# Performance work log

Hardware: AMD Instinct MI355X
Metric: run time of the kernel (lower is better)

## Reference

```python
import jax, jax.numpy as jnp
import numpy as np

GRID_SIZE = 5
SPLINE_ORDER = 3
GRID_RANGE = (-1.0, 1.0)
LAYERS = [1024, 1024, 1024]
BATCH = 8192
LN_EPS = 1e-5


def _make_grid(in_features):
    h = (GRID_RANGE[1] - GRID_RANGE[0]) / GRID_SIZE
    n = GRID_SIZE + 2 * SPLINE_ORDER + 1  # 12 knots
    g = jnp.linspace(GRID_RANGE[0] - h * SPLINE_ORDER,
                     GRID_RANGE[1] + h * SPLINE_ORDER, n, dtype=jnp.float32)
    return jnp.broadcast_to(g, (in_features, n))


def setup_inputs() -> dict:
    key = jax.random.key(0)
    ks = jax.random.split(key, 8)
    n_layers = len(LAYERS) - 1
    d_in, d_out = LAYERS[0], LAYERS[1]  # square layers -> stackable params
    coeff = GRID_SIZE + SPLINE_ORDER  # 8
    # kaiming_uniform_(nonlinearity='linear'): bound = sqrt(3) * (1/sqrt(fan_in))
    bw_bound = float(np.sqrt(3.0) / np.sqrt(d_in))
    sw_bound = float(np.sqrt(3.0) / np.sqrt(d_in * coeff))
    x = jax.random.normal(ks[0], (BATCH, d_in), dtype=jnp.float32)
    base_w = jax.random.uniform(ks[1], (n_layers, d_out, d_in), jnp.float32, -bw_bound, bw_bound)
    spline_w = jax.random.uniform(ks[2], (n_layers, d_out, d_in, coeff), jnp.float32, -sw_bound, sw_bound)
    ln_g = jnp.ones((n_layers, d_out), jnp.float32)
    ln_b = jnp.zeros((n_layers, d_out), jnp.float32)
    prelu_a = jnp.full((n_layers,), 0.25, jnp.float32)
    grid = jnp.stack([_make_grid(d_in) for _ in range(n_layers)])  # [L, in, 12]
    return {"x": x, "base_w": base_w, "spline_w": spline_w,
            "ln_g": ln_g, "ln_b": ln_b, "prelu_a": prelu_a, "grid": grid}


def _bspline_bases(x, g):
    """Cox-de Boor recursion. x: [B, in], g: [in, n_knots] -> [B, in, G+order]."""
    xu = x[..., None]  # [B, in, 1]
    bases = ((xu >= g[:, :-1]) & (xu < g[:, 1:])).astype(x.dtype)  # [B, in, 11]
    for k in range(1, SPLINE_ORDER + 1):
        left = g[:, :-(k + 1)]
        right = g[:, k:-1]
        delta = jnp.where(right == left, jnp.ones_like(right), right - left)
        bases = ((xu - left) / delta * bases[..., :-1]
                 + (g[:, k + 1:] - xu) / (g[:, k + 1:] - g[:, 1:-k]) * bases[..., 1:])
    return bases  # [B, in, 8]


def kan_forward(x, base_w, spline_w, ln_g, ln_b, prelu_a, grid):
    n_layers = base_w.shape[0]
    for i in range(n_layers):
        base_out = jnp.matmul(jax.nn.gelu(x, approximate=False), base_w[i].T)  # [B, out]
        bases = _bspline_bases(x, grid[i])  # [B, in, 8]
        spline_out = jnp.matmul(bases.reshape(x.shape[0], -1),
                                spline_w[i].reshape(spline_w.shape[1], -1).T)  # [B, out]
        h = base_out + spline_out
        mu = jnp.mean(h, axis=-1, keepdims=True)
        var = jnp.var(h, axis=-1, keepdims=True)  # biased, matches torch LayerNorm
        h = (h - mu) * jax.lax.rsqrt(var + LN_EPS) * ln_g[i] + ln_b[i]
        x = jnp.where(h >= 0, h, prelu_a[i] * h)  # PReLU (scalar slope per layer)
    return x


def reference(x, base_w, spline_w, ln_g, ln_b, prelu_a, grid):
    return kan_forward(x, base_w, spline_w, ln_g, ln_b, prelu_a, grid)
```

## Files before the change

### kernel.cpp

```cpp
#include <hip/hip_runtime.h>
#include <hip/hip_bf16.h>
#include <cstdint>
#include <cstddef>

typedef __bf16 bf16_t;
typedef __bf16 bf16x8 __attribute__((ext_vector_type(8)));
typedef __bf16 bf16x4 __attribute__((ext_vector_type(4)));
typedef float  f32x4  __attribute__((ext_vector_type(4)));

#define DIM    1024
#define NCOEF  8
#define KTOT   (DIM + DIM * NCOEF)
#define NKNOT  12
#define BATCH  8192
#define LN_EPS 1e-5f

__device__ __forceinline__ float gelu_exact(float x) {
    return 0.5f * x * (1.0f + erff(x * 0.70710678118654752440f));
}

__device__ __forceinline__ void gl_lds16(const void* g, void* l) {
    __builtin_amdgcn_global_load_lds(
        (const __attribute__((address_space(1))) unsigned int*)(uintptr_t)g,
        (__attribute__((address_space(3))) unsigned int*)(uintptr_t)l, 16, 0, 0);
}

__device__ __forceinline__ uint64_t pack4bf(float a, float b, float c, float d) {
    union { bf16_t h[4]; uint64_t q; } u;
    u.h[0] = (bf16_t)a; u.h[1] = (bf16_t)b; u.h[2] = (bf16_t)c; u.h[3] = (bf16_t)d;
    return u.q;
}

__device__ __forceinline__ void spline8(float x, float g0, float invh,
                                        uint64_t& lo, uint64_t& hi) {
    float u = (x - g0) * invh;
    float jf = floorf(u);
    int j = (int)jf;
    float f = u - jf;
    float f2 = f * f, f3 = f2 * f;
    float om = 1.0f - f, om2 = om * om;
    float w0 = om2 * om * (1.0f / 6.0f);
    float w3 = f3 * (1.0f / 6.0f);
    float w1 = fmaf(0.5f, f3, 2.0f / 3.0f) - f2;
    float w2 = 1.0f - w0 - w1 - w3;
    uint64_t W64 = pack4bf(w0, w1, w2, w3);
    if (!(u >= 0.0f && u < 11.0f)) W64 = 0;
    int sh = (j - 3) * 16;
    if (sh >= 0) {
        int s = sh & 63;
        uint64_t loW = W64 << s;
        uint64_t hiW = s ? (W64 >> (64 - s)) : 0ull;
        lo = (sh < 64) ? loW : 0ull;
        hi = (sh < 64) ? hiW : loW;
    } else {
        lo = W64 >> (-sh);
        hi = 0ull;
    }
}

__global__ void pack_w(const float* __restrict__ bw, const float* __restrict__ sw,
                       bf16_t* __restrict__ W) {
    int idx = blockIdx.x * 256 + threadIdx.x;
    bf16_t* wrow = W + (size_t)(idx >> 10) * KTOT;
    int j = idx & 1023;
    wrow[j] = (bf16_t)bw[idx];
    const float4* sp = (const float4*)(sw + (size_t)idx * NCOEF);
    float4 s0 = sp[0], s1 = sp[1];
    bf16x8 v;
    v[0] = (bf16_t)s0.x; v[1] = (bf16_t)s0.y; v[2] = (bf16_t)s0.z; v[3] = (bf16_t)s0.w;
    v[4] = (bf16_t)s1.x; v[5] = (bf16_t)s1.y; v[6] = (bf16_t)s1.z; v[7] = (bf16_t)s1.w;
    *(bf16x8*)(wrow + DIM + j * NCOEF) = v;
}

__global__ void prep_A(const float* __restrict__ x, bf16_t* __restrict__ A,
                       const float* __restrict__ gp, int R) {
    const int t = threadIdx.x;
    const float g0 = gp[0];
    const float invh = 1.0f / (gp[1] - gp[0]);
    for (int row = blockIdx.x; row < R; row += gridDim.x) {
        f32x4 v = *(const f32x4*)(x + (size_t)row * DIM + t * 4);
        bf16_t* Ar = A + (size_t)row * KTOT;
        bf16x4 ge;
#pragma unroll
        for (int k = 0; k < 4; k++) ge[k] = (bf16_t)gelu_exact(v[k]);
        *(bf16x4*)(Ar + t * 4) = ge;
#pragma unroll
        for (int k = 0; k < 4; k++) {
            uint64_t lo, hi;
            union { uint64_t u[2]; uint4 q; } o;
            spline8(v[k], g0, invh, lo, hi);
            o.u[0] = lo; o.u[1] = hi;
            *(uint4*)(Ar + DIM + (t * 4 + k) * NCOEF) = o.q;
        }
    }
}


#define STR2(x) #x
#define GATEV(N) asm volatile("s_waitcnt vmcnt(" STR2(N) ")" ::: "memory");
#define LGKM(N)  asm volatile("s_waitcnt lgkmcnt(" STR2(N) ")" ::: "memory");
#define BAR() { __builtin_amdgcn_s_barrier(); asm volatile("" ::: "memory"); }

#define EA(i) ea##i
#define EB(i) eb##i
#define OA(i) oa##i
#define OB(i) ob##i

#define MF_ROWX(I, A_, CB) \
    acc[I][0] = __builtin_amdgcn_mfma_f32_16x16x32_bf16(A_, CB(0), acc[I][0], 0, 0, 0); \
    acc[I][1] = __builtin_amdgcn_mfma_f32_16x16x32_bf16(A_, CB(1), acc[I][1], 0, 0, 0); \
    acc[I][2] = __builtin_amdgcn_mfma_f32_16x16x32_bf16(A_, CB(2), acc[I][2], 0, 0, 0); \
    acc[I][3] = __builtin_amdgcn_mfma_f32_16x16x32_bf16(A_, CB(3), acc[I][3], 0, 0, 0);

#define TILE(T, S, SN, SP, STG, GATESTMT, RD, WAITB, CA, CB, NA, NB) { \
     \
    if (STG) { \
      gl_lds16(Ag0 + (size_t)((T) + 3) * 32, ldsA + (SP) * 8192 + tid * 8); \
      gl_lds16(Ag1 + (size_t)((T) + 3) * 32, ldsA + (SP) * 8192 + 4096 + tid * 8); } \
    { const bf16_t* Ab_ = ldsA + (S) * 8192 + aOff; \
      CA(4) = *(const bf16x8*)(Ab_ + 2048); CA(5) = *(const bf16x8*)(Ab_ + 2560); \
      CA(6) = *(const bf16x8*)(Ab_ + 3072); CA(7) = *(const bf16x8*)(Ab_ + 3584); } \
    LGKM(4) \
    __builtin_amdgcn_sched_barrier(0); \
    __builtin_amdgcn_s_setprio(1); \
    MF_ROWX(0, CA(0), CB) MF_ROWX(1, CA(1), CB) \
    MF_ROWX(2, CA(2), CB) MF_ROWX(3, CA(3), CB) \
    __builtin_amdgcn_s_setprio(0); \
     \
    if (STG) { \
      gl_lds16(Bg0 + (size_t)((T) + 3) * 32, ldsB + (SP) * 8192 + tid * 8); \
      gl_lds16(Bg1 + (size_t)((T) + 3) * 32, ldsB + (SP) * 8192 + 4096 + tid * 8); } \
    GATESTMT \
    if (RD) { \
      BAR() \
      const bf16_t* An_ = ldsA + (SN) * 8192 + aOff; \
      const bf16_t* Bn_ = ldsB + (SN) * 8192 + bOff; \
      NA(0) = *(const bf16x8*)(An_);        NA(1) = *(const bf16x8*)(An_ + 512); \
      NA(2) = *(const bf16x8*)(An_ + 1024); NA(3) = *(const bf16x8*)(An_ + 1536); \
      NB(0) = *(const bf16x8*)(Bn_);        NB(1) = *(const bf16x8*)(Bn_ + 512); \
      NB(2) = *(const bf16x8*)(Bn_ + 1024); NB(3) = *(const bf16x8*)(Bn_ + 1536); } \
    WAITB \
    __builtin_amdgcn_sched_barrier(0); \
    __builtin_amdgcn_s_setprio(1); \
    MF_ROWX(4, CA(4), CB) MF_ROWX(5, CA(5), CB) \
    MF_ROWX(6, CA(6), CB) MF_ROWX(7, CA(7), CB) \
    __builtin_amdgcn_s_setprio(0); \
    BAR() \
}

#define PSTAGE(T, S) \
    gl_lds16(Ag0 + (size_t)(T) * 32, ldsA + (S) * 8192 + tid * 8); \
    gl_lds16(Ag1 + (size_t)(T) * 32, ldsA + (S) * 8192 + 4096 + tid * 8); \
    gl_lds16(Bg0 + (size_t)(T) * 32, ldsB + (S) * 8192 + tid * 8); \
    gl_lds16(Bg1 + (size_t)(T) * 32, ldsB + (S) * 8192 + 4096 + tid * 8);

template<int NTK>
__global__ __launch_bounds__(512, 2) void gemm_ab(
    const bf16_t* __restrict__ A,
    const bf16_t* __restrict__ W,
    float* __restrict__ C,
    int mmask, int mshift, int rows) {
    __shared__ __align__(16) bf16_t lds[65536];
    bf16_t* __restrict__ ldsA = lds;
    bf16_t* __restrict__ ldsB = lds + 32768;

    const int tid = threadIdx.x;
    const int l = tid & 63, wv = tid >> 6;
    const int wm = wv >> 2, wn = wv & 3;

    const int chunk = gridDim.x >> 3;
    const int bid = blockIdx.x;
    const int wg = (bid & 7) * chunk + (bid >> 3);
    const int bm = wg & mmask;
    const int bn = (wg >> mshift) & 3;
    const int ks = wg >> (mshift + 2);
    const int row0 = bm << 8, col0 = bn << 8;
    const int koff0 = ks * (NTK * 32);

    const int srow = tid >> 2;
    const int slc = (tid & 3) ^ ((srow >> 1) & 3);
    const bf16_t* __restrict__ Ag0 = A + (size_t)(row0 + srow) * KTOT + koff0 + slc * 8;
    const bf16_t* __restrict__ Ag1 = Ag0 + (size_t)128 * KTOT;
    const bf16_t* __restrict__ Bg0 = W + (size_t)(col0 + srow) * KTOT + koff0 + slc * 8;
    const bf16_t* __restrict__ Bg1 = Bg0 + (size_t)128 * KTOT;

    const int l15 = l & 15;
    const int pc = (l >> 4) ^ ((l15 >> 1) & 3);
    const int aOff = (wm * 128 + l15) * 32 + pc * 8;
    const int bOff = (wn * 64 + l15) * 32 + pc * 8;

    f32x4 acc[8][4] = {};
    bf16x8 ea0, ea1, ea2, ea3, ea4, ea5, ea6, ea7, eb0, eb1, eb2, eb3;
    bf16x8 oa0, oa1, oa2, oa3, oa4, oa5, oa6, oa7, ob0, ob1, ob2, ob3;

    PSTAGE(0, 0)
    PSTAGE(1, 1)
    PSTAGE(2, 2)
    GATEV(8)
    BAR()
    {
        const bf16_t* An_ = ldsA + aOff;
        const bf16_t* Bn_ = ldsB + bOff;
        ea0 = *(const bf16x8*)(An_);        ea1 = *(const bf16x8*)(An_ + 512);
        ea2 = *(const bf16x8*)(An_ + 1024); ea3 = *(const bf16x8*)(An_ + 1536);
        eb0 = *(const bf16x8*)(Bn_);        eb1 = *(const bf16x8*)(Bn_ + 512);
        eb2 = *(const bf16x8*)(Bn_ + 1024); eb3 = *(const bf16x8*)(Bn_ + 1536);
    }

#pragma unroll 1
    for (int t = 0; t < NTK - 4; t += 4) {
        TILE(t + 0, 0, 1, 3, 1, GATEV(8), 1, LGKM(8), EA, EB, OA, OB)
        TILE(t + 1, 1, 2, 0, 1, GATEV(8), 1, LGKM(8), OA, OB, EA, EB)
        TILE(t + 2, 2, 3, 1, 1, GATEV(8), 1, LGKM(8), EA, EB, OA, OB)
        TILE(t + 3, 3, 0, 2, 1, GATEV(8), 1, LGKM(8), OA, OB, EA, EB)
    }
    TILE(NTK - 4, 0, 1, 3, 1, GATEV(8), 1, LGKM(8), EA, EB, OA, OB)
    TILE(NTK - 3, 1, 2, 0, 0, GATEV(4), 1, LGKM(8), OA, OB, EA, EB)
    TILE(NTK - 2, 2, 3, 1, 0, GATEV(0), 1, LGKM(8), EA, EB, OA, OB)
    TILE(NTK - 1, 3, 0, 2, 0, GATEV(0), 0, LGKM(0), OA, OB, EA, EB)

    float* __restrict__ Cp = C + (size_t)ks * rows * DIM;
    const int r0 = row0 + wm * 128 + (l >> 4) * 4;
    const int c0 = col0 + wn * 64 + l15;
#pragma unroll
    for (int i = 0; i < 8; i++)
#pragma unroll
        for (int j = 0; j < 4; j++)
#pragma unroll
            for (int r = 0; r < 4; r++)
                Cp[(size_t)(r0 + i * 16 + r) * DIM + c0 + j * 16] = acc[i][j][r];
}

__global__ void ln_mid_A(const float* __restrict__ h, int rows, int ksplit,
                         const float* __restrict__ g_ln, const float* __restrict__ b_ln,
                         const float* __restrict__ pa, bf16_t* __restrict__ A,
                         const float* __restrict__ gp) {
    const int tid = threadIdx.x;
    const int w = tid >> 6, l = tid & 63;
    const float a = pa[0];
    const float g0 = gp[0];
    const float invh = 1.0f / (gp[1] - gp[0]);
    __shared__ float rs[4], rq[4];
    for (int row = blockIdx.x; row < rows; row += gridDim.x) {
        f32x4 v = {0.0f, 0.0f, 0.0f, 0.0f};
        for (int ks = 0; ks < ksplit; ks++)
            v += *(const f32x4*)(h + ((size_t)ks * rows + row) * DIM + tid * 4);
        float s = v[0] + v[1] + v[2] + v[3];
        float q = v[0] * v[0] + v[1] * v[1] + v[2] * v[2] + v[3] * v[3];
#pragma unroll
        for (int o = 32; o > 0; o >>= 1) { s += __shfl_xor(s, o); q += __shfl_xor(q, o); }
        if (l == 0) { rs[w] = s; rq[w] = q; }
        __syncthreads();
        s = rs[0] + rs[1] + rs[2] + rs[3];
        q = rq[0] + rq[1] + rq[2] + rq[3];
        __syncthreads();
        float mean = s * (1.0f / DIM);
        float var = q * (1.0f / DIM) - mean * mean;
        float rstd = rsqrtf(var + LN_EPS);
        bf16_t* Ar = A + (size_t)row * KTOT;
        bf16x4 ge;
#pragma unroll
        for (int c = 0; c < 4; c++) {
            int col = tid * 4 + c;
            float yv = (v[c] - mean) * rstd * g_ln[col] + b_ln[col];
            yv = (yv >= 0.0f) ? yv : a * yv;
            ge[c] = (bf16_t)gelu_exact(yv);
            uint64_t lo, hi;
            union { uint64_t u[2]; uint4 qv; } o;
            spline8(yv, g0, invh, lo, hi);
            o.u[0] = lo; o.u[1] = hi;
            *(uint4*)(Ar + DIM + (size_t)col * NCOEF) = o.qv;
        }
        *(bf16x4*)(Ar + tid * 4) = ge;
    }
}

__global__ void ln_out(const float* __restrict__ h, int rows, int ksplit,
                       const float* __restrict__ g_ln, const float* __restrict__ b_ln,
                       const float* __restrict__ pa, float* __restrict__ out) {
    const int tid = threadIdx.x;
    const int w = tid >> 6, l = tid & 63;
    const float a = pa[0];
    __shared__ float rs[4], rq[4];
    for (int row = blockIdx.x; row < rows; row += gridDim.x) {
        f32x4 v = {0.0f, 0.0f, 0.0f, 0.0f};
        for (int ks = 0; ks < ksplit; ks++)
            v += *(const f32x4*)(h + ((size_t)ks * rows + row) * DIM + tid * 4);
        float s = v[0] + v[1] + v[2] + v[3];
        float q = v[0] * v[0] + v[1] * v[1] + v[2] * v[2] + v[3] * v[3];
#pragma unroll
        for (int o = 32; o > 0; o >>= 1) { s += __shfl_xor(s, o); q += __shfl_xor(q, o); }
        if (l == 0) { rs[w] = s; rq[w] = q; }
        __syncthreads();
        s = rs[0] + rs[1] + rs[2] + rs[3];
        q = rq[0] + rq[1] + rq[2] + rq[3];
        __syncthreads();
        float mean = s * (1.0f / DIM);
        float var = q * (1.0f / DIM) - mean * mean;
        float rstd = rsqrtf(var + LN_EPS);
        f32x4 o4;
#pragma unroll
        for (int c = 0; c < 4; c++) {
            int col = tid * 4 + c;
            float yv = (v[c] - mean) * rstd * g_ln[col] + b_ln[col];
            o4[c] = (yv >= 0.0f) ? yv : a * yv;
        }
        *(f32x4*)(out + (size_t)row * DIM + tid * 4) = o4;
    }
}

extern "C" void kernel_launch(void* const* d_in, const int* in_sizes, int n_in,
                              void* d_out, int out_size, void* d_ws, size_t ws_size,
                              hipStream_t stream) {
    const float* x    = (const float*)d_in[0];
    const float* bw   = (const float*)d_in[1];
    const float* sw   = (const float*)d_in[2];
    const float* ln_g = (const float*)d_in[3];
    const float* ln_b = (const float*)d_in[4];
    const float* pa   = (const float*)d_in[5];
    const float* gridK = (const float*)d_in[6];
    float* out = (float*)d_out;

    const size_t wbytes = (size_t)2 * DIM * KTOT * sizeof(bf16_t);
    int R = 8192, ksplit = 2;
    for (;;) {
        size_t need = wbytes + (size_t)R * KTOT * 2 + (size_t)ksplit * R * DIM * 4;
        if (need <= ws_size || R == 512) break;
        R >>= 1;
        int mt = R / 256;
        ksplit = (mt >= 32) ? 2 : (mt >= 16) ? 4 : 8;
    }
    int mtiles = R / 256;
    int mshift = 0; while ((1 << mshift) < mtiles) mshift++;
    int mmask = mtiles - 1;
    int grid = mtiles * 4 * ksplit;
    int lng = (R >= 2048) ? 2048 : R;

    char* wsc = (char*)d_ws;
    bf16_t* Wbuf = (bf16_t*)wsc;
    bf16_t* Abuf = (bf16_t*)(wsc + wbytes);
    float*  hbuf = (float*)(wsc + wbytes + (size_t)R * KTOT * 2);

    pack_w<<<(2 * DIM * DIM) / 256, 256, 0, stream>>>(bw, sw, Wbuf);

    auto launch_gemm = [&](const bf16_t* Wl, hipStream_t st) {
        if (ksplit == 2)
            gemm_ab<144><<<grid, 512, 0, st>>>(Abuf, Wl, hbuf, mmask, mshift, R);
        else if (ksplit == 4)
            gemm_ab<72><<<grid, 512, 0, st>>>(Abuf, Wl, hbuf, mmask, mshift, R);
        else
            gemm_ab<36><<<grid, 512, 0, st>>>(Abuf, Wl, hbuf, mmask, mshift, R);
    };

    const int nslab = BATCH / R;
    for (int sidx = 0; sidx < nslab; sidx++) {
        const size_t row0 = (size_t)sidx * R;
        const float* x0 = x + row0 * DIM;
        prep_A<<<lng, 256, 0, stream>>>(x0, Abuf, gridK, R);
        launch_gemm(Wbuf, stream);
        ln_mid_A<<<lng, 256, 0, stream>>>(hbuf, R, ksplit, ln_g, ln_b, pa,
                                          Abuf, gridK + DIM * NKNOT);
        launch_gemm(Wbuf + (size_t)DIM * KTOT, stream);
        ln_out<<<lng, 256, 0, stream>>>(hbuf, R, ksplit, ln_g + DIM, ln_b + DIM,
                                        pa + 1, out + row0 * DIM);
    }
}
```

Baseline: 574.8 us.

## Restructure GEMM main loop into K=64 double-buffered 8-phase ping-pong schedule

```diff
diff --git a/kernel.cpp b/kernel.cpp
--- a/kernel.cpp
+++ b/kernel.cpp
@@ -98,61 +98,78 @@
 
 #define STR2(x) #x
 #define GATEV(N) asm volatile("s_waitcnt vmcnt(" STR2(N) ")" ::: "memory");
-#define LGKM(N)  asm volatile("s_waitcnt lgkmcnt(" STR2(N) ")" ::: "memory");
+#define LGKM0    asm volatile("s_waitcnt lgkmcnt(0)" ::: "memory");
 #define BAR() { __builtin_amdgcn_s_barrier(); asm volatile("" ::: "memory"); }
 
-#define EA(i) ea##i
-#define EB(i) eb##i
-#define OA(i) oa##i
-#define OB(i) ob##i
-
-#define MF_ROWX(I, A_, CB) \
-    acc[I][0] = __builtin_amdgcn_mfma_f32_16x16x32_bf16(A_, CB(0), acc[I][0], 0, 0, 0); \
-    acc[I][1] = __builtin_amdgcn_mfma_f32_16x16x32_bf16(A_, CB(1), acc[I][1], 0, 0, 0); \
-    acc[I][2] = __builtin_amdgcn_mfma_f32_16x16x32_bf16(A_, CB(2), acc[I][2], 0, 0, 0); \
-    acc[I][3] = __builtin_amdgcn_mfma_f32_16x16x32_bf16(A_, CB(3), acc[I][3], 0, 0, 0);
-
-#define TILE(T, S, SN, SP, STG, GATESTMT, RD, WAITB, CA, CB, NA, NB) { \
-     \
-    if (STG) { \
-      gl_lds16(Ag0 + (size_t)((T) + 3) * 32, ldsA + (SP) * 8192 + tid * 8); \
-      gl_lds16(Ag1 + (size_t)((T) + 3) * 32, ldsA + (SP) * 8192 + 4096 + tid * 8); } \
-    { const bf16_t* Ab_ = ldsA + (S) * 8192 + aOff; \
-      CA(4) = *(const bf16x8*)(Ab_ + 2048); CA(5) = *(const bf16x8*)(Ab_ + 2560); \
-      CA(6) = *(const bf16x8*)(Ab_ + 3072); CA(7) = *(const bf16x8*)(Ab_ + 3584); } \
-    LGKM(4) \
-    __builtin_amdgcn_sched_barrier(0); \
-    __builtin_amdgcn_s_setprio(1); \
-    MF_ROWX(0, CA(0), CB) MF_ROWX(1, CA(1), CB) \
-    MF_ROWX(2, CA(2), CB) MF_ROWX(3, CA(3), CB) \
-    __builtin_amdgcn_s_setprio(0); \
-     \
-    if (STG) { \
-      gl_lds16(Bg0 + (size_t)((T) + 3) * 32, ldsB + (SP) * 8192 + tid * 8); \
-      gl_lds16(Bg1 + (size_t)((T) + 3) * 32, ldsB + (SP) * 8192 + 4096 + tid * 8); } \
-    GATESTMT \
-    if (RD) { \
-      BAR() \
-      const bf16_t* An_ = ldsA + (SN) * 8192 + aOff; \
-      const bf16_t* Bn_ = ldsB + (SN) * 8192 + bOff; \
-      NA(0) = *(const bf16x8*)(An_);        NA(1) = *(const bf16x8*)(An_ + 512); \
-      NA(2) = *(const bf16x8*)(An_ + 1024); NA(3) = *(const bf16x8*)(An_ + 1536); \
-      NB(0) = *(const bf16x8*)(Bn_);        NB(1) = *(const bf16x8*)(Bn_ + 512); \
-      NB(2) = *(const bf16x8*)(Bn_ + 1024); NB(3) = *(const bf16x8*)(Bn_ + 1536); } \
-    WAITB \
-    __builtin_amdgcn_sched_barrier(0); \
-    __builtin_amdgcn_s_setprio(1); \
-    MF_ROWX(4, CA(4), CB) MF_ROWX(5, CA(5), CB) \
-    MF_ROWX(6, CA(6), CB) MF_ROWX(7, CA(7), CB) \
-    __builtin_amdgcn_s_setprio(0); \
-    BAR() \
-}
-
-#define PSTAGE(T, S) \
-    gl_lds16(Ag0 + (size_t)(T) * 32, ldsA + (S) * 8192 + tid * 8); \
-    gl_lds16(Ag1 + (size_t)(T) * 32, ldsA + (S) * 8192 + 4096 + tid * 8); \
-    gl_lds16(Bg0 + (size_t)(T) * 32, ldsB + (S) * 8192 + tid * 8); \
-    gl_lds16(Bg1 + (size_t)(T) * 32, ldsB + (S) * 8192 + 4096 + tid * 8);
+#define RD_A(DST, BO, G) { \
+    const bf16_t* p_ = ldsA + (BO) + aOffBase + (G) * 2048; \
+    DST[0][0] = *(const bf16x8*)(p_);        DST[1][0] = *(const bf16x8*)(p_ + 512); \
+    DST[2][0] = *(const bf16x8*)(p_ + 1024); DST[3][0] = *(const bf16x8*)(p_ + 1536); \
+    DST[0][1] = *(const bf16x8*)(p_ + 4096); DST[1][1] = *(const bf16x8*)(p_ + 4608); \
+    DST[2][1] = *(const bf16x8*)(p_ + 5120); DST[3][1] = *(const bf16x8*)(p_ + 5632); }
+
+#define RD_B(DST, BO, CG) { \
+    const bf16_t* p_ = ldsB + (BO) + bOffBase + (CG) * 1024; \
+    DST[0][0] = *(const bf16x8*)(p_);        DST[1][0] = *(const bf16x8*)(p_ + 512); \
+    DST[0][1] = *(const bf16x8*)(p_ + 4096); DST[1][1] = *(const bf16x8*)(p_ + 4608); }
+
+#define STG_A(TILE, HALF) { \
+    const bf16_t* s_ = AgS + (size_t)(HALF) * (128 * (size_t)KTOT) + (size_t)(TILE) * 64; \
+    bf16_t* d_ = ldsA + (((TILE) & 1) * 16384) + (HALF) * 8192 + tid * 8; \
+    gl_lds16(s_, d_); gl_lds16(s_ + 32, d_ + 4096); }
+
+#define STG_B(TILE, HALF) { \
+    const bf16_t* s_ = BgS + (size_t)(HALF) * (128 * (size_t)KTOT) + (size_t)(TILE) * 64; \
+    bf16_t* d_ = ldsB + (((TILE) & 1) * 16384) + (HALF) * 8192 + tid * 8; \
+    gl_lds16(s_, d_); gl_lds16(s_ + 32, d_ + 4096); }
+
+#define MFQ(G, CG, AS, BS) { \
+    _Pragma("unroll") \
+    for (int ks_ = 0; ks_ < 2; ks_++) \
+    _Pragma("unroll") \
+    for (int fr_ = 0; fr_ < 4; fr_++) \
+    _Pragma("unroll") \
+    for (int cf_ = 0; cf_ < 2; cf_++) \
+        acc[(G) * 4 + fr_][(CG) * 2 + cf_] = __builtin_amdgcn_mfma_f32_16x16x32_bf16( \
+            AS[fr_][ks_], BS[cf_][ks_], acc[(G) * 4 + fr_][(CG) * 2 + cf_], 0, 0, 0); }
+
+#define PHX(MF, ENDG) \
+    BAR() LGKM0 __builtin_amdgcn_sched_barrier(0); \
+    __builtin_amdgcn_s_setprio(1); MF __builtin_amdgcn_s_setprio(0); \
+    ENDG BAR()
+
+#define ITER8(T, S12, S34, S56, S78, G4T, G8T) { \
+     \
+    RD_A(Ar0, 0, 0) RD_B(Bc0, 0, 0) \
+    if (S12) { STG_B((T) + 1, 0) } \
+    PHX(MFQ(0, 0, Ar0, Bc0), ;) \
+     \
+    RD_A(Ar1, 0, 1) \
+    if (S12) { STG_B((T) + 1, 1) } \
+    PHX(MFQ(1, 0, Ar1, Bc0), ;) \
+     \
+    RD_B(Bc1, 0, 1) \
+    if (S34) { STG_A((T) + 2, 0) } \
+    PHX(MFQ(1, 1, Ar1, Bc1), ;) \
+     \
+    if (S34) { STG_A((T) + 2, 1) } \
+    PHX(MFQ(0, 1, Ar0, Bc1), G4T) \
+     \
+    RD_A(Ar0, 16384, 0) RD_B(Bc0, 16384, 0) \
+    if (S56) { STG_B((T) + 2, 0) } \
+    PHX(MFQ(0, 0, Ar0, Bc0), ;) \
+     \
+    RD_A(Ar1, 16384, 1) \
+    if (S56) { STG_B((T) + 2, 1) } \
+    PHX(MFQ(1, 0, Ar1, Bc0), ;) \
+     \
+    RD_B(Bc1, 16384, 1) \
+    if (S78) { STG_A((T) + 3, 0) } \
+    PHX(MFQ(1, 1, Ar1, Bc1), ;) \
+     \
+    if (S78) { STG_A((T) + 3, 1) } \
+    PHX(MFQ(0, 1, Ar0, Bc1), G8T) \
+}
 
 template<int NTK>
 __global__ __launch_bounds__(512, 2) void gemm_ab(
@@ -175,49 +192,33 @@
     const int bn = (wg >> mshift) & 3;
     const int ks = wg >> (mshift + 2);
     const int row0 = bm << 8, col0 = bn << 8;
-    const int koff0 = ks * (NTK * 32);
+    const int koff0 = ks * (NTK * 64);
 
     const int srow = tid >> 2;
-    const int slc = (tid & 3) ^ ((srow >> 1) & 3);
-    const bf16_t* __restrict__ Ag0 = A + (size_t)(row0 + srow) * KTOT + koff0 + slc * 8;
-    const bf16_t* __restrict__ Ag1 = Ag0 + (size_t)128 * KTOT;
-    const bf16_t* __restrict__ Bg0 = W + (size_t)(col0 + srow) * KTOT + koff0 + slc * 8;
-    const bf16_t* __restrict__ Bg1 = Bg0 + (size_t)128 * KTOT;
+    const int schunk = (tid & 3) ^ ((srow >> 1) & 3);
+    const bf16_t* __restrict__ AgS = A + (size_t)(row0 + srow) * KTOT + koff0 + schunk * 8;
+    const bf16_t* __restrict__ BgS = W + (size_t)(col0 + srow) * KTOT + koff0 + schunk * 8;
 
     const int l15 = l & 15;
     const int pc = (l >> 4) ^ ((l15 >> 1) & 3);
-    const int aOff = (wm * 128 + l15) * 32 + pc * 8;
-    const int bOff = (wn * 64 + l15) * 32 + pc * 8;
+    const int aOffBase = wm * 8192 + l15 * 32 + pc * 8;
+    const int bOffBase = (wn >> 1) * 8192 + (wn & 1) * 2048 + l15 * 32 + pc * 8;
 
     f32x4 acc[8][4] = {};
-    bf16x8 ea0, ea1, ea2, ea3, ea4, ea5, ea6, ea7, eb0, eb1, eb2, eb3;
-    bf16x8 oa0, oa1, oa2, oa3, oa4, oa5, oa6, oa7, ob0, ob1, ob2, ob3;
-
-    PSTAGE(0, 0)
-    PSTAGE(1, 1)
-    PSTAGE(2, 2)
-    GATEV(8)
+    bf16x8 Ar0[4][2], Ar1[4][2], Bc0[2][2], Bc1[2][2];
+
+    STG_A(0, 0) STG_A(0, 1)
+    STG_B(0, 0) STG_B(0, 1)
+    STG_A(1, 0) STG_A(1, 1)
+    GATEV(4)
     BAR()
-    {
-        const bf16_t* An_ = ldsA + aOff;
-        const bf16_t* Bn_ = ldsB + bOff;
-        ea0 = *(const bf16x8*)(An_);        ea1 = *(const bf16x8*)(An_ + 512);
-        ea2 = *(const bf16x8*)(An_ + 1024); ea3 = *(const bf16x8*)(An_ + 1536);
-        eb0 = *(const bf16x8*)(Bn_);        eb1 = *(const bf16x8*)(Bn_ + 512);
-        eb2 = *(const bf16x8*)(Bn_ + 1024); eb3 = *(const bf16x8*)(Bn_ + 1536);
-    }
 
 #pragma unroll 1
-    for (int t = 0; t < NTK - 4; t += 4) {
-        TILE(t + 0, 0, 1, 3, 1, GATEV(8), 1, LGKM(8), EA, EB, OA, OB)
-        TILE(t + 1, 1, 2, 0, 1, GATEV(8), 1, LGKM(8), OA, OB, EA, EB)
-        TILE(t + 2, 2, 3, 1, 1, GATEV(8), 1, LGKM(8), EA, EB, OA, OB)
-        TILE(t + 3, 3, 0, 2, 1, GATEV(8), 1, LGKM(8), OA, OB, EA, EB)
-    }
-    TILE(NTK - 4, 0, 1, 3, 1, GATEV(8), 1, LGKM(8), EA, EB, OA, OB)
-    TILE(NTK - 3, 1, 2, 0, 0, GATEV(4), 1, LGKM(8), OA, OB, EA, EB)
-    TILE(NTK - 2, 2, 3, 1, 0, GATEV(0), 1, LGKM(8), EA, EB, OA, OB)
-    TILE(NTK - 1, 3, 0, 2, 0, GATEV(0), 0, LGKM(0), OA, OB, EA, EB)
+    for (int i = 0; i < NTK / 2 - 1; i++) {
+        const int T = 2 * i;
+        ITER8(T, 1, 1, 1, 1, GATEV(4), GATEV(4))
+    }
+    ITER8(NTK - 2, 1, 0, 0, 0, GATEV(0), ;)
 
     float* __restrict__ Cp = C + (size_t)ks * rows * DIM;
     const int r0 = row0 + wm * 128 + (l >> 4) * 4;
@@ -345,11 +346,11 @@
 
     auto launch_gemm = [&](const bf16_t* Wl, hipStream_t st) {
         if (ksplit == 2)
-            gemm_ab<144><<<grid, 512, 0, st>>>(Abuf, Wl, hbuf, mmask, mshift, R);
+            gemm_ab<72><<<grid, 512, 0, st>>>(Abuf, Wl, hbuf, mmask, mshift, R);
         else if (ksplit == 4)
-            gemm_ab<72><<<grid, 512, 0, st>>>(Abuf, Wl, hbuf, mmask, mshift, R);
+            gemm_ab<36><<<grid, 512, 0, st>>>(Abuf, Wl, hbuf, mmask, mshift, R);
         else
-            gemm_ab<36><<<grid, 512, 0, st>>>(Abuf, Wl, hbuf, mmask, mshift, R);
+            gemm_ab<18><<<grid, 512, 0, st>>>(Abuf, Wl, hbuf, mmask, mshift, R);
     };
 
     const int nslab = BATCH / R;
```

New measurement: 512.2 us. 10.9% less time.
